# Kernel tuning notes

Hardware: AMD Instinct MI355X
Metric: run time of the kernel (lower is better)

## Reference

```python
import jax, jax.numpy as jnp
import numpy as np

B, C, H, W = 4, 256, 64, 64
EMB = C // 8  # embedding_channels = inChannels // k


def _conv1x1(x, w, b):
    # x: [B, Cin, H, W], w: [Cout, Cin], b: [Cout] -> [B, Cout, H, W]
    return jnp.einsum('oi,bihw->bohw', w, x) + b[None, :, None, None]


def setup_inputs() -> dict:
    key = jax.random.key(0)
    ks = jax.random.split(key, 10)
    s = 0.05
    return {
        'x': jax.random.normal(ks[0], (B, C, H, W), dtype=jnp.float32),
        'key_w': jax.random.normal(ks[1], (EMB, C), dtype=jnp.float32) * s,
        'key_b': jax.random.normal(ks[2], (EMB,), dtype=jnp.float32) * s,
        'query_w': jax.random.normal(ks[3], (EMB, C), dtype=jnp.float32) * s,
        'query_b': jax.random.normal(ks[4], (EMB,), dtype=jnp.float32) * s,
        'value_w': jax.random.normal(ks[5], (EMB, C), dtype=jnp.float32) * s,
        'value_b': jax.random.normal(ks[6], (EMB,), dtype=jnp.float32) * s,
        'att_w': jax.random.normal(ks[7], (C, EMB), dtype=jnp.float32) * s,
        'att_b': jax.random.normal(ks[8], (C,), dtype=jnp.float32) * s,
        'gamma': jnp.zeros((), dtype=jnp.float32),
    }


def reference(x, key_w, key_b, query_w, query_b, value_w, value_b, att_w, att_b, gamma):
    b, c, h, w = x.shape
    n = h * w
    f = _conv1x1(x, key_w, key_b).reshape(b, -1, n)    # [B, E, N]
    g = _conv1x1(x, query_w, query_b).reshape(b, -1, n)  # [B, E, N]
    hh = _conv1x1(x, value_w, value_b).reshape(b, -1, n)  # [B, E, N]
    # s[b,i,j] = sum_e f[b,e,i] * g[b,e,j]
    s = jnp.einsum('bei,bej->bij', f, g)  # [B, N, N]
    # NOTE: softmax over dim=1 (the i / key-index axis), NOT the last dim
    beta = jax.nn.softmax(s, axis=1)
    v = jnp.einsum('bei,bij->bej', hh, beta).reshape(b, -1, h, w)  # [B, E, H, W]
    o = _conv1x1(v, att_w, att_b)  # [B, C, H, W]
    y = gamma * o + x
    return (y, o)
```

## Files before the change

### kernel.cpp

```cpp
#include <hip/hip_runtime.h>
#include <hip/hip_bf16.h>
#include <math.h>

#define BB 4
#define CC 256
#define NN 4096
#define EE 32

typedef __attribute__((ext_vector_type(8))) short bf16x8;
typedef __attribute__((ext_vector_type(4))) float f32x4;
typedef __attribute__((ext_vector_type(16))) float f32x16;
typedef __attribute__((ext_vector_type(2))) unsigned uint32x2_t;

__device__ inline unsigned short f2bf(float x) {
    union { __hip_bfloat16 h; unsigned short u; } cv;
    cv.h = __float2bfloat16(x);
    return cv.u;
}
__device__ inline unsigned pk2(float lo, float hi) {
    return ((unsigned)f2bf(hi) << 16) | (unsigned)f2bf(lo);
}
__device__ inline float fexp2(float x) { return __builtin_amdgcn_exp2f(x); }
__device__ inline unsigned cvtpk(float lo, float hi) {
    unsigned r;
    asm("v_cvt_pk_bf16_f32 %0, %1, %2" : "=v"(r) : "v"(lo), "v"(hi));
    return r;
}
__device__ inline float bflo(unsigned u) {
    union { unsigned v; float f; } c; c.v = u << 16; return c.f;
}
__device__ inline float bfhi(unsigned u) {
    union { unsigned v; float f; } c; c.v = u & 0xFFFF0000u; return c.f;
}

__global__ __launch_bounds__(256) void wcvt_kernel(
    const float* __restrict__ kw, const float* __restrict__ kb,
    const float* __restrict__ qw, const float* __restrict__ qb,
    const float* __restrict__ vw, const float* __restrict__ vb,
    __hip_bfloat16* __restrict__ wB, float* __restrict__ bB)
{
    int r = blockIdx.x;
    int t = threadIdx.x;
    int rr = r & 31;
    const float* src; float scale = 1.f;
    if (r < 32)      src = kw;
    else if (r < 64) { src = qw; scale = 1.44269504f; }
    else             src = vw;
    if (t < 64) {
        float4 v = *(const float4*)(src + rr * 256 + t * 4);
        uint2 p;
        p.x = pk2(v.x * scale, v.y * scale);
        p.y = pk2(v.z * scale, v.w * scale);
        *(uint2*)((unsigned short*)wB + r * 256 + t * 4) = p;
    }
    if (r == 0 && t >= 64 && t < 160) {
        int e = t - 64;
        const float* bs = (e < 32) ? kb : ((e < 64) ? qb : vb);
        float sc = (e >= 32 && e < 64) ? 1.44269504f : 1.f;
        bB[e] = bs[e & 31] * sc;
    }
}

__global__ __launch_bounds__(256) void proj_kernel(
    const float* __restrict__ x,
    const __hip_bfloat16* __restrict__ wB, const float* __restrict__ bB,
    __hip_bfloat16* __restrict__ fT, __hip_bfloat16* __restrict__ gT,
    __hip_bfloat16* __restrict__ hT)
{
    __shared__ unsigned xs[32][132];
    int b     = blockIdx.x >> 7;
    int ibase = (blockIdx.x & 127) << 5;
    int wv    = threadIdx.x >> 6;
    int l     = threadIdx.x & 63;
    int il    = l & 31;
    int pg    = (wv << 1) | (l >> 5);

    const float* xb = x + (size_t)b * CC * NN + ibase + il;
#pragma unroll
    for (int j = 0; j < 16; ++j) {
        int p = pg + (j << 3);
        float lo = xb[(size_t)(2 * p) * NN];
        float hi = xb[(size_t)(2 * p + 1) * NN];
        xs[il][p] = pk2(lo, hi);
    }
    __syncthreads();

    int q15  = l & 15, g = l >> 4;
    int isub = wv & 1, eh = wv >> 1;
    int irow = (isub << 4) + q15;
    const __hip_bfloat16* w0 = wB + ((size_t)(eh * 48) + q15) * 256;

    f32x4 a0 = {0,0,0,0}, a1 = {0,0,0,0}, a2 = {0,0,0,0};
#pragma unroll
    for (int kk = 0; kk < 8; ++kk) {
        bf16x8 Bf = *(const bf16x8*)&xs[irow][kk * 16 + 4 * g];
        int co = kk * 32 + 8 * g;
        bf16x8 A0 = *(const bf16x8*)(w0 + co);
        bf16x8 A1 = *(const bf16x8*)(w0 + 16 * 256 + co);
        bf16x8 A2 = *(const bf16x8*)(w0 + 32 * 256 + co);
        a0 = __builtin_amdgcn_mfma_f32_16x16x32_bf16(A0, Bf, a0, 0, 0, 0);
        a1 = __builtin_amdgcn_mfma_f32_16x16x32_bf16(A1, Bf, a1, 0, 0, 0);
        a2 = __builtin_amdgcn_mfma_f32_16x16x32_bf16(A2, Bf, a2, 0, 0, 0);
    }

    int ig = ibase + irow;
    auto emit = [&](f32x4 acc, int T) {
        float4 bb = *(const float4*)(bB + T * 16 + 4 * g);
        float d0 = acc[0] + bb.x, d1 = acc[1] + bb.y;
        float d2 = acc[2] + bb.z, d3 = acc[3] + bb.w;
        if (T < 4) {
            __hip_bfloat16* dst = (T < 2) ? fT : gT;
            int eoff = ((T & 1) << 4) + 4 * g;
            uint2 pq; pq.x = pk2(d0, d1); pq.y = pk2(d2, d3);
            *(uint2*)((unsigned short*)dst + ((size_t)b * NN + ig) * EE + eoff) = pq;
        } else {
            unsigned short* dst = (unsigned short*)hT;
            int e  = ((T - 4) << 4) + 4 * g;
            int kt = ig >> 5, kk2 = ig & 31;
            size_t base = ((size_t)(b * 128 + kt) * 32 + e) * 32 + kk2;
            dst[base]       = f2bf(d0);
            dst[base + 32]  = f2bf(d1);
            dst[base + 64]  = f2bf(d2);
            dst[base + 96]  = f2bf(d3);
        }
    };
    emit(a0, eh * 3 + 0);
    emit(a1, eh * 3 + 1);
    emit(a2, eh * 3 + 2);
}

__global__ __launch_bounds__(1024, 4) void attn_kernel(
    const __hip_bfloat16* __restrict__ fT,
    const __hip_bfloat16* __restrict__ gT,
    const __hip_bfloat16* __restrict__ hT,
    float* __restrict__ vT)
{
    int b     = blockIdx.x >> 6;
    int ibase = (blockIdx.x & 63) << 6;
    int wv    = threadIdx.x >> 6;
    int lane  = threadIdx.x & 63;
    int q     = lane & 31;
    int h     = lane >> 5;

    const __hip_bfloat16* fb = fT + (size_t)b * NN * EE;
    const __hip_bfloat16* gb = gT + (size_t)b * NN * EE;
    const __hip_bfloat16* hb = hT + (size_t)b * NN * EE + q * 32 + 8 * h;

    bf16x8 Qa0 = *(const bf16x8*)(gb + (size_t)(ibase + q) * EE + 8 * h);
    bf16x8 Qa1 = *(const bf16x8*)(gb + (size_t)(ibase + q) * EE + 16 + 8 * h);
    bf16x8 Qb0 = *(const bf16x8*)(gb + (size_t)(ibase + 32 + q) * EE + 8 * h);
    bf16x8 Qb1 = *(const bf16x8*)(gb + (size_t)(ibase + 32 + q) * EE + 16 + 8 * h);

    float lA = 0.f, lB = 0.f;
    f32x16 OA = {0,0,0,0,0,0,0,0,0,0,0,0,0,0,0,0};
    f32x16 OB = {0,0,0,0,0,0,0,0,0,0,0,0,0,0,0,0};
    const f32x16 z16 = {0,0,0,0,0,0,0,0,0,0,0,0,0,0,0,0};

    int k0 = wv * 256;
    bf16x8 K0 = *(const bf16x8*)(fb + (size_t)(k0 + q) * EE + 8 * h);
    bf16x8 K1 = *(const bf16x8*)(fb + (size_t)(k0 + q) * EE + 16 + 8 * h);

    for (int c = 0; c < 8; ++c) {
        int kn = (k0 + 32) & (NN - 1);
        bf16x8 nK0 = *(const bf16x8*)(fb + (size_t)(kn + q) * EE + 8 * h);
        bf16x8 nK1 = *(const bf16x8*)(fb + (size_t)(kn + q) * EE + 16 + 8 * h);
        bf16x8 V0  = *(const bf16x8*)(hb + (size_t)k0 * 32);
        bf16x8 V1  = *(const bf16x8*)(hb + (size_t)k0 * 32 + 16);

        __builtin_amdgcn_s_setprio(1);
        f32x16 SA = __builtin_amdgcn_mfma_f32_32x32x16_bf16(K0, Qa0, z16, 0, 0, 0);
        SA = __builtin_amdgcn_mfma_f32_32x32x16_bf16(K1, Qa1, SA, 0, 0, 0);
        __builtin_amdgcn_s_setprio(0);

        {
            float p[16];
#pragma unroll
            for (int r = 0; r < 16; ++r) p[r] = fexp2(SA[r]);
            lA += ((p[0]+p[1])+(p[2]+p[3])) + ((p[4]+p[5])+(p[6]+p[7]))
                + ((p[8]+p[9])+(p[10]+p[11])) + ((p[12]+p[13])+(p[14]+p[15]));
            unsigned j0 = cvtpk(p[0], p[1]),   j1 = cvtpk(p[2], p[3]);
            unsigned j2 = cvtpk(p[4], p[5]),   j3 = cvtpk(p[6], p[7]);
            unsigned j4 = cvtpk(p[8], p[9]),   j5 = cvtpk(p[10], p[11]);
            unsigned j6 = cvtpk(p[12], p[13]), j7 = cvtpk(p[14], p[15]);
            uint32x2_t sA2 = __builtin_amdgcn_permlane32_swap(j0, j2, false, false);
            uint32x2_t sB2 = __builtin_amdgcn_permlane32_swap(j1, j3, false, false);
            union { unsigned u[4]; bf16x8 v; } P1;
            P1.u[0] = sA2.x; P1.u[1] = sB2.x; P1.u[2] = sA2.y; P1.u[3] = sB2.y;
            uint32x2_t sC2 = __builtin_amdgcn_permlane32_swap(j4, j6, false, false);
            uint32x2_t sD2 = __builtin_amdgcn_permlane32_swap(j5, j7, false, false);
            union { unsigned u[4]; bf16x8 v; } P2;
            P2.u[0] = sC2.x; P2.u[1] = sD2.x; P2.u[2] = sC2.y; P2.u[3] = sD2.y;
            __builtin_amdgcn_s_setprio(1);
            OA = __builtin_amdgcn_mfma_f32_32x32x16_bf16(V0, P1.v, OA, 0, 0, 0);
            OA = __builtin_amdgcn_mfma_f32_32x32x16_bf16(V1, P2.v, OA, 0, 0, 0);
            __builtin_amdgcn_s_setprio(0);
        }

        __builtin_amdgcn_s_setprio(1);
        f32x16 SB = __builtin_amdgcn_mfma_f32_32x32x16_bf16(K0, Qb0, z16, 0, 0, 0);
        SB = __builtin_amdgcn_mfma_f32_32x32x16_bf16(K1, Qb1, SB, 0, 0, 0);
        __builtin_amdgcn_s_setprio(0);

        {
            float p[16];
#pragma unroll
            for (int r = 0; r < 16; ++r) p[r] = fexp2(SB[r]);
            lB += ((p[0]+p[1])+(p[2]+p[3])) + ((p[4]+p[5])+(p[6]+p[7]))
                + ((p[8]+p[9])+(p[10]+p[11])) + ((p[12]+p[13])+(p[14]+p[15]));
            unsigned j0 = cvtpk(p[0], p[1]),   j1 = cvtpk(p[2], p[3]);
            unsigned j2 = cvtpk(p[4], p[5]),   j3 = cvtpk(p[6], p[7]);
            unsigned j4 = cvtpk(p[8], p[9]),   j5 = cvtpk(p[10], p[11]);
            unsigned j6 = cvtpk(p[12], p[13]), j7 = cvtpk(p[14], p[15]);
            uint32x2_t sA2 = __builtin_amdgcn_permlane32_swap(j0, j2, false, false);
            uint32x2_t sB2 = __builtin_amdgcn_permlane32_swap(j1, j3, false, false);
            union { unsigned u[4]; bf16x8 v; } P1;
            P1.u[0] = sA2.x; P1.u[1] = sB2.x; P1.u[2] = sA2.y; P1.u[3] = sB2.y;
            uint32x2_t sC2 = __builtin_amdgcn_permlane32_swap(j4, j6, false, false);
            uint32x2_t sD2 = __builtin_amdgcn_permlane32_swap(j5, j7, false, false);
            union { unsigned u[4]; bf16x8 v; } P2;
            P2.u[0] = sC2.x; P2.u[1] = sD2.x; P2.u[2] = sC2.y; P2.u[3] = sD2.y;
            __builtin_amdgcn_s_setprio(1);
            OB = __builtin_amdgcn_mfma_f32_32x32x16_bf16(V0, P1.v, OB, 0, 0, 0);
            OB = __builtin_amdgcn_mfma_f32_32x32x16_bf16(V1, P2.v, OB, 0, 0, 0);
            __builtin_amdgcn_s_setprio(0);
        }

        K0 = nK0; K1 = nK1;
        k0 = kn;
    }

    __shared__ unsigned sOp[16][64][17];
    __shared__ float    slx[16][64][2];
    slx[wv][lane][0] = lA;
    slx[wv][lane][1] = lB;
#pragma unroll
    for (int r = 0; r < 8; ++r) {
        sOp[wv][lane][r]     = cvtpk(OA[2*r], OA[2*r+1]);
        sOp[wv][lane][8 + r] = cvtpk(OB[2*r], OB[2*r+1]);
    }
    __syncthreads();

    if (wv < 2) {
        int set = wv;
        float L = 0.f;
        float Of[16];
#pragma unroll
        for (int r = 0; r < 16; ++r) Of[r] = 0.f;
#pragma unroll
        for (int w = 0; w < 16; ++w) {
            L += slx[w][lane][set];
#pragma unroll
            for (int r = 0; r < 8; ++r) {
                unsigned u = sOp[w][lane][set * 8 + r];
                Of[2*r]   += bflo(u);
                Of[2*r+1] += bfhi(u);
            }
        }
        L += __shfl_xor(L, 32, 64);
        float inv = 1.f / L;
        float* vp = vT + ((size_t)b * NN + ibase + set * 32 + q) * EE;
#pragma unroll
        for (int gi = 0; gi < 4; ++gi) {
            f32x4 ov;
#pragma unroll
            for (int r = 0; r < 4; ++r) ov[r] = Of[4 * gi + r] * inv;
            *(f32x4*)(vp + 8 * gi + 4 * h) = ov;
        }
    }
}

__global__ __launch_bounds__(256) void out_kernel(
    const float* __restrict__ vT, const float* __restrict__ aw,
    const float* __restrict__ ab, const float* __restrict__ x,
    const float* __restrict__ gamma_p,
    float* __restrict__ y, float* __restrict__ o)
{
    int blk    = blockIdx.x;
    int csplit = blk & 15;
    int itile  = (blk >> 4) & 15;
    int b      = blk >> 8;
    int i      = itile * 256 + threadIdx.x;
    float gm   = gamma_p[0];

    const float4* vp4 = (const float4*)(vT + ((size_t)b * NN + i) * EE);
    float vr[EE];
#pragma unroll
    for (int u = 0; u < 8; ++u) {
        float4 t = vp4[u];
        vr[4*u+0] = t.x; vr[4*u+1] = t.y; vr[4*u+2] = t.z; vr[4*u+3] = t.w;
    }

    int co0 = csplit * 16;
#pragma unroll
    for (int co = co0; co < co0 + 16; ++co) {
        float s = ab[co];
#pragma unroll
        for (int e = 0; e < EE; ++e)
            s = fmaf(aw[co * EE + e], vr[e], s);
        size_t idx = ((size_t)b * CC + co) * NN + i;
        o[idx] = s;
        y[idx] = fmaf(gm, s, x[idx]);
    }
}

extern "C" void kernel_launch(void* const* d_in, const int* in_sizes, int n_in,
                              void* d_out, int out_size, void* d_ws, size_t ws_size,
                              hipStream_t stream)
{
    const float* x  = (const float*)d_in[0];
    const float* kw = (const float*)d_in[1];
    const float* kb = (const float*)d_in[2];
    const float* qw = (const float*)d_in[3];
    const float* qb = (const float*)d_in[4];
    const float* vw = (const float*)d_in[5];
    const float* vb = (const float*)d_in[6];
    const float* aw = (const float*)d_in[7];
    const float* ab = (const float*)d_in[8];
    const float* gm = (const float*)d_in[9];

    float* y = (float*)d_out;
    float* o = y + (size_t)BB * CC * NN;

    float*          vT = (float*)d_ws;
    float*          bB = vT + (size_t)BB * NN * EE;
    __hip_bfloat16* wB = (__hip_bfloat16*)(bB + 128);
    __hip_bfloat16* fT = wB + 96 * 256;
    __hip_bfloat16* gT = fT + (size_t)BB * NN * EE;
    __hip_bfloat16* hT = gT + (size_t)BB * NN * EE;

    wcvt_kernel<<<96, 256, 0, stream>>>(kw, kb, qw, qb, vw, vb, wB, bB);
    proj_kernel<<<BB * (NN / 32), 256, 0, stream>>>(x, wB, bB, fT, gT, hT);
    attn_kernel<<<BB * (NN / 64), 1024, 0, stream>>>(fT, gT, hT, vT);
    out_kernel<<<BB * 16 * 16, 256, 0, stream>>>(vT, aw, ab, x, gm, y, o);
}
```

Baseline: 62.13 us.

## Remap block indices across XCDs, vectorize x loads, prefetch V in attention

All three kernels now remap blockIdx so that consecutive blocks spread over batches, likely to keep each batch's data together per XCD or L2 slice. The projection kernel loads x with float4 reads along the spatial axis instead of scalar strided loads. The attention kernel software-pipelines the V tile loads one iteration ahead, like the existing K prefetch. Together these aim to cut load latency and improve cache locality, at the cost of more live registers and a changed LDS write pattern that may cause bank conflicts.

```diff
diff --git a/kernel.cpp b/kernel.cpp
--- a/kernel.cpp
+++ b/kernel.cpp
@@ -68,23 +68,29 @@
     __hip_bfloat16* __restrict__ hT)
 {
     __shared__ unsigned xs[32][132];
-    int b     = blockIdx.x >> 7;
-    int ibase = (blockIdx.x & 127) << 5;
-    int wv    = threadIdx.x >> 6;
-    int l     = threadIdx.x & 63;
-    int il    = l & 31;
-    int pg    = (wv << 1) | (l >> 5);
-
-    const float* xb = x + (size_t)b * CC * NN + ibase + il;
-#pragma unroll
-    for (int j = 0; j < 16; ++j) {
-        int p = pg + (j << 3);
-        float lo = xb[(size_t)(2 * p) * NN];
-        float hi = xb[(size_t)(2 * p + 1) * NN];
-        xs[il][p] = pk2(lo, hi);
+    int blk   = blockIdx.x;
+    int b     = (blk & 7) >> 1;
+    int itile = ((blk >> 3) << 1) | (blk & 1);
+    int ibase = itile << 5;
+
+    int t   = threadIdx.x;
+    int ig4 = (t & 7) * 4;
+    int crw = t >> 3;
+    const float* xb = x + (size_t)b * CC * NN + ibase;
+#pragma unroll
+    for (int it = 0; it < 4; ++it) {
+        int cp = it * 32 + crw;
+        float4 fa = *(const float4*)(xb + (size_t)(2 * cp) * NN + ig4);
+        float4 fc = *(const float4*)(xb + (size_t)(2 * cp + 1) * NN + ig4);
+        xs[ig4 + 0][cp] = pk2(fa.x, fc.x);
+        xs[ig4 + 1][cp] = pk2(fa.y, fc.y);
+        xs[ig4 + 2][cp] = pk2(fa.z, fc.z);
+        xs[ig4 + 3][cp] = pk2(fa.w, fc.w);
     }
     __syncthreads();
 
+    int wv = threadIdx.x >> 6;
+    int l  = threadIdx.x & 63;
     int q15  = l & 15, g = l >> 4;
     int isub = wv & 1, eh = wv >> 1;
     int irow = (isub << 4) + q15;
@@ -135,8 +141,9 @@
     const __hip_bfloat16* __restrict__ hT,
     float* __restrict__ vT)
 {
-    int b     = blockIdx.x >> 6;
-    int ibase = (blockIdx.x & 63) << 6;
+    int blk   = blockIdx.x;
+    int b     = (blk & 7) >> 1;
+    int ibase = (((blk >> 3) << 1) | (blk & 1)) << 6;
     int wv    = threadIdx.x >> 6;
     int lane  = threadIdx.x & 63;
     int q     = lane & 31;
@@ -159,13 +166,15 @@
     int k0 = wv * 256;
     bf16x8 K0 = *(const bf16x8*)(fb + (size_t)(k0 + q) * EE + 8 * h);
     bf16x8 K1 = *(const bf16x8*)(fb + (size_t)(k0 + q) * EE + 16 + 8 * h);
+    bf16x8 V0 = *(const bf16x8*)(hb + (size_t)k0 * 32);
+    bf16x8 V1 = *(const bf16x8*)(hb + (size_t)k0 * 32 + 16);
 
     for (int c = 0; c < 8; ++c) {
         int kn = (k0 + 32) & (NN - 1);
         bf16x8 nK0 = *(const bf16x8*)(fb + (size_t)(kn + q) * EE + 8 * h);
         bf16x8 nK1 = *(const bf16x8*)(fb + (size_t)(kn + q) * EE + 16 + 8 * h);
-        bf16x8 V0  = *(const bf16x8*)(hb + (size_t)k0 * 32);
-        bf16x8 V1  = *(const bf16x8*)(hb + (size_t)k0 * 32 + 16);
+        bf16x8 nV0 = *(const bf16x8*)(hb + (size_t)kn * 32);
+        bf16x8 nV1 = *(const bf16x8*)(hb + (size_t)kn * 32 + 16);
 
         __builtin_amdgcn_s_setprio(1);
         f32x16 SA = __builtin_amdgcn_mfma_f32_32x32x16_bf16(K0, Qa0, z16, 0, 0, 0);
@@ -225,7 +234,7 @@
             __builtin_amdgcn_s_setprio(0);
         }
 
-        K0 = nK0; K1 = nK1;
+        K0 = nK0; K1 = nK1; V0 = nV0; V1 = nV1;
         k0 = kn;
     }
 
@@ -276,9 +285,10 @@
     float* __restrict__ y, float* __restrict__ o)
 {
     int blk    = blockIdx.x;
-    int csplit = blk & 15;
-    int itile  = (blk >> 4) & 15;
-    int b      = blk >> 8;
+    int b      = (blk & 7) >> 1;
+    int rest   = ((blk >> 3) << 1) | (blk & 1);
+    int csplit = rest & 15;
+    int itile  = rest >> 4;
     int i      = itile * 256 + threadIdx.x;
     float gm   = gamma_p[0];
 
```

Result: slower. 68.19 us (+9.8%).
